# Performance work log

Measured on AMD Instinct MI355X. Metric: run time of the kernel, lower is better.

## Reference

```python
import jax, jax.numpy as jnp
import numpy as np

N, E, G, D, FIN, L, ELAB = 150000, 600000, 8192, 128, 16, 4, 500000
BN_EPS = 1e-5


def _bn(h, g, b, rm, rv):
    # eval-mode BatchNorm1d with running stats
    return (h - rm) * g * jax.lax.rsqrt(rv + BN_EPS) + b


def _pool_max(h, batch):
    # global_max_pool; empty segments -> 0 (instead of -inf)
    p = jax.ops.segment_max(h, batch, num_segments=G)
    return jnp.where(jnp.isneginf(p), 0.0, p)


def setup_inputs() -> dict:
    key = jax.random.key(0)
    ks = jax.random.split(key, 24)
    s_in = 1.0 / np.sqrt(FIN)
    s_d = 1.0 / np.sqrt(D)
    inp = {
        "x": jax.random.normal(ks[0], (N, FIN), jnp.float32),
        "edge_index": jax.random.randint(ks[1], (2, E), 0, N, jnp.int32),
        "batch": jnp.sort(jax.random.randint(ks[2], (N,), 0, G, jnp.int32)),
        "edge_index_labeled": jax.random.randint(ks[3], (2, ELAB), 0, G, jnp.int32),
        "edge_label": jax.random.randint(ks[4], (ELAB,), 0, 2, jnp.int32),
        # initial node encoder + initial linear (num_classes == emb_sizes == D)
        "enc_W": jax.random.normal(ks[5], (FIN, D), jnp.float32) * s_in,
        "enc_b": jnp.zeros((D,), jnp.float32),
        "init_W": jax.random.normal(ks[6], (D, D), jnp.float32) * s_d,
        "init_b": jnp.zeros((D,), jnp.float32),
        # per-layer GIN params (stacked over L layers)
        "gin_eps": jnp.zeros((L,), jnp.float32),
        "W1": jax.random.normal(ks[7], (L, D, D), jnp.float32) * s_d,
        "b1": jnp.zeros((L, D), jnp.float32),
        "g1": jnp.ones((L, D), jnp.float32),
        "be1": jnp.zeros((L, D), jnp.float32),
        "rm1": jnp.zeros((L, D), jnp.float32),
        "rv1": jnp.ones((L, D), jnp.float32),
        "W2": jax.random.normal(ks[8], (L, D, D), jnp.float32) * s_d,
        "b2": jnp.zeros((L, D), jnp.float32),
        "g2": jnp.ones((L, D), jnp.float32),
        "be2": jnp.zeros((L, D), jnp.float32),
        "rm2": jnp.zeros((L, D), jnp.float32),
        "rv2": jnp.ones((L, D), jnp.float32),
        # per-layer linear applied to pooled features
        "lin_W": jax.random.normal(ks[9], (L, D, D), jnp.float32) * s_d,
        "lin_b": jnp.zeros((L, D), jnp.float32),
        # layer_post_mp: ReLU -> Linear(D,D) -> ReLU -> Linear(D,1)
        "post_W1": jax.random.normal(ks[10], (D, D), jnp.float32) * s_d,
        "post_b1": jnp.zeros((D,), jnp.float32),
        "post_W2": jax.random.normal(ks[11], (D, 1), jnp.float32) * s_d,
        "post_b2": jnp.zeros((1,), jnp.float32),
    }
    return inp


def reference(x, edge_index, batch, edge_index_labeled, edge_label,
              enc_W, enc_b, init_W, init_b, gin_eps,
              W1, b1, g1, be1, rm1, rv1,
              W2, b2, g2, be2, rm2, rv2,
              lin_W, lin_b, post_W1, post_b1, post_W2, post_b2):
    src, dst = edge_index[0], edge_index[1]

    # initial MLP (node encoder) -> [N, D]
    x_feat = x @ enc_W + enc_b

    # out = dropout(pool(initial_linear(x_feat)))  (dropout = identity, eval)
    out = _pool_max(x_feat @ init_W + init_b, batch)  # [G, D]

    for i in range(L):
        # GINConv: mlp((1 + eps) * x + sum_{j in N(i)} x_j)
        agg = jax.ops.segment_sum(x_feat[src], dst, num_segments=N)  # [N, D]
        h = (1.0 + gin_eps[i]) * x_feat + agg
        h = jax.nn.relu(_bn(h @ W1[i] + b1[i], g1[i], be1[i], rm1[i], rv1[i]))
        x_feat = jax.nn.relu(_bn(h @ W2[i] + b2[i], g2[i], be2[i], rm2[i], rv2[i]))
        # out += dropout(linear(pool(x_feat)))
        out = out + (_pool_max(x_feat, batch) @ lin_W[i] + lin_b[i])

    # layer_post_mp: ReLU -> Linear -> ReLU -> Linear(D,1)
    out = jax.nn.relu(out)
    out = jax.nn.relu(out @ post_W1 + post_b1)
    out = out @ post_W2 + post_b2  # [G, 1]

    # _apply_index gather + dot-product decode
    pred_pairs = out[edge_index_labeled]  # [2, ELAB, 1]
    pred = jnp.sum(pred_pairs[0] * pred_pairs[1], axis=-1)  # [ELAB]
    return pred, edge_label
```

## Files before the change

kernel.cpp:

```cpp
#include <hip/hip_runtime.h>

#define NN 150000
#define NP 150016
#define NE 600000
#define NG 8192
#define DD 128
#define FINN 16
#define NL 4
#define NEL 500000
#define BN_EPS 1e-5f
#define NB_SCAN 147

typedef __attribute__((ext_vector_type(8))) short bf16x8;
typedef __attribute__((ext_vector_type(4))) float f32x4;
typedef __attribute__((ext_vector_type(2))) float f32x2;

__device__ inline short bfr(float x) {
    unsigned u = __builtin_bit_cast(unsigned, x);
    unsigned r = u + 0x7fffu + ((u >> 16) & 1u);
    return (short)(r >> 16);
}
__device__ inline float bf2f(short h) {
    return __builtin_bit_cast(float, ((unsigned)(unsigned short)h) << 16);
}

__global__ __launch_bounds__(256) void enc_kernel(const float* __restrict__ x,
                                                  const float* __restrict__ W,
                                                  const float* __restrict__ b,
                                                  float* __restrict__ out) {
    int t = threadIdx.x;
    int c4 = (t & 31) * 4;
    float4 wreg[16];
#pragma unroll
    for (int k = 0; k < 16; k++) wreg[k] = *(const float4*)&W[k * DD + c4];
    float4 bias = *(const float4*)&b[c4];
    int rbase = blockIdx.x * 128 + (t >> 5);
#pragma unroll
    for (int it = 0; it < 16; it++) {
        int row = rbase + it * 8;
        if (row >= NN) break;
        const float4* xr = (const float4*)(x + (size_t)row * FINN);
        float4 x0 = xr[0], x1 = xr[1], x2 = xr[2], x3 = xr[3];
        float xs[16] = {x0.x, x0.y, x0.z, x0.w, x1.x, x1.y, x1.z, x1.w,
                        x2.x, x2.y, x2.z, x2.w, x3.x, x3.y, x3.z, x3.w};
        float4 acc = bias;
#pragma unroll
        for (int k = 0; k < 16; k++) {
            acc.x += xs[k] * wreg[k].x;
            acc.y += xs[k] * wreg[k].y;
            acc.z += xs[k] * wreg[k].z;
            acc.w += xs[k] * wreg[k].w;
        }
        *(float4*)&out[(size_t)row * DD + c4] = acc;
    }
}

__global__ void prep_w_kernel(const float* __restrict__ initW, const float* __restrict__ W1,
                              const float* __restrict__ W2, bf16x8* __restrict__ Wph,
                              bf16x8* __restrict__ Wpl) {
    int tid = blockIdx.x * 256 + threadIdx.x;
    if (tid >= 9 * 2048) return;
    int mat = tid >> 11;
    int rem = tid & 2047;
    int kk = rem >> 9;
    int c = (rem >> 6) & 7;
    int lane = rem & 63;
    const float* Wm;
    if (mat == 0) Wm = initW;
    else if (mat <= 4) Wm = W1 + (size_t)(mat - 1) * DD * DD;
    else Wm = W2 + (size_t)(mat - 5) * DD * DD;
    int col = c * 16 + (lane & 15);
    int kbase = kk * 32 + (lane >> 4) * 8;
    bf16x8 oh, ol;
#pragma unroll
    for (int j = 0; j < 8; j++) {
        float v = Wm[(size_t)(kbase + j) * DD + col];
        short h = bfr(v);
        oh[j] = h;
        ol[j] = bfr(v - bf2f(h));
    }
    Wph[tid] = oh;
    Wpl[tid] = ol;
}

__global__ void prep_scb_kernel(const float* __restrict__ initb,
                                const float* __restrict__ b1, const float* __restrict__ g1,
                                const float* __restrict__ be1, const float* __restrict__ rm1,
                                const float* __restrict__ rv1,
                                const float* __restrict__ b2, const float* __restrict__ g2,
                                const float* __restrict__ be2, const float* __restrict__ rm2,
                                const float* __restrict__ rv2,
                                float* __restrict__ sc, float* __restrict__ bb) {
    int tid = blockIdx.x * 256 + threadIdx.x;
    if (tid >= 9 * DD) return;
    int mat = tid >> 7, d = tid & 127;
    float s, o;
    if (mat == 0) {
        s = 1.f;
        o = initb[d];
    } else {
        const float *b_, *g_, *be_, *rm_, *rv_;
        int i;
        if (mat <= 4) { i = mat - 1; b_ = b1; g_ = g1; be_ = be1; rm_ = rm1; rv_ = rv1; }
        else          { i = mat - 5; b_ = b2; g_ = g2; be_ = be2; rm_ = rm2; rv_ = rv2; }
        float t = g_[i * DD + d] * rsqrtf(rv_[i * DD + d] + BN_EPS);
        s = t;
        o = (b_[i * DD + d] - rm_[i * DD + d]) * t + be_[i * DD + d];
    }
    sc[tid] = s;
    bb[tid] = o;
}

__global__ void zero_int_kernel(int* __restrict__ p, int n) {
    int i = blockIdx.x * 256 + threadIdx.x;
    if (i < n) p[i] = 0;
}

__global__ void hist_kernel(const int* __restrict__ dst, int* __restrict__ deg) {
    int e = blockIdx.x * 256 + threadIdx.x;
    if (e < NE) atomicAdd(&deg[dst[e]], 1);
}

__global__ void scan_reduce_kernel(const int* __restrict__ deg, int* __restrict__ bsum) {
    __shared__ int s[256];
    int b = blockIdx.x, t = threadIdx.x;
    int base = b * 1024 + t * 4;
    int v = 0;
#pragma unroll
    for (int i = 0; i < 4; i++) {
        int idx = base + i;
        if (idx < NN) v += deg[idx];
    }
    s[t] = v;
    __syncthreads();
    for (int off = 128; off > 0; off >>= 1) {
        if (t < off) s[t] += s[t + off];
        __syncthreads();
    }
    if (t == 0) bsum[b] = s[0];
}

__global__ void scan_mid_kernel(const int* __restrict__ bsum, int* __restrict__ boff,
                                int* __restrict__ rowptrN) {
    __shared__ int s[256];
    int t = threadIdx.x;
    int v = (t < NB_SCAN) ? bsum[t] : 0;
    s[t] = v;
    __syncthreads();
    for (int off = 1; off < 256; off <<= 1) {
        int u = (t >= off) ? s[t - off] : 0;
        __syncthreads();
        s[t] += u;
        __syncthreads();
    }
    if (t < NB_SCAN) boff[t] = s[t] - v;
    if (t == 255) *rowptrN = s[255];
}

__global__ void scan_final_kernel(const int* __restrict__ deg, const int* __restrict__ boff,
                                  int* __restrict__ rowptr) {
    __shared__ int s[256];
    int b = blockIdx.x, t = threadIdx.x;
    int base = b * 1024 + t * 4;
    int v[4];
    int sum = 0;
#pragma unroll
    for (int i = 0; i < 4; i++) {
        int idx = base + i;
        v[i] = (idx < NN) ? deg[idx] : 0;
        sum += v[i];
    }
    s[t] = sum;
    __syncthreads();
    int my = sum;
    for (int off = 1; off < 256; off <<= 1) {
        int u = (t >= off) ? s[t - off] : 0;
        __syncthreads();
        s[t] += u;
        __syncthreads();
    }
    int excl = s[t] - my + boff[b];
#pragma unroll
    for (int i = 0; i < 4; i++) {
        int idx = base + i;
        if (idx < NN) rowptr[idx] = excl;
        excl += v[i];
    }
}

__global__ void copy_int_kernel(const int* __restrict__ a, int* __restrict__ b, int n) {
    int i = blockIdx.x * 256 + threadIdx.x;
    if (i < n) b[i] = a[i];
}

__global__ void fill_kernel(const int* __restrict__ src, const int* __restrict__ dst,
                            int* cursor, int* __restrict__ csr_src) {
    int e = blockIdx.x * 256 + threadIdx.x;
    if (e >= NE) return;
    int p = atomicAdd(&cursor[dst[e]], 1);
    csr_src[p] = src[e];
}

__global__ void gstart_kernel(const int* __restrict__ batch, int* __restrict__ gstart) {
    int n = blockIdx.x * 256 + threadIdx.x;
    if (n >= NN) return;
    int b = batch[n];
    int prev = (n == 0) ? -1 : batch[n - 1];
    for (int g = prev + 1; g <= b; g++) gstart[g] = n;
    if (n == NN - 1) {
        for (int g = b + 1; g <= NG; g++) gstart[g] = NN;
    }
}

__global__ __launch_bounds__(256) void agg_kernel(const float* __restrict__ A,
                                                  const int* __restrict__ rowptr,
                                                  const int* __restrict__ csr_src,
                                                  const float* __restrict__ gin_eps,
                                                  int li, unsigned short* __restrict__ Bh) {
    int n = __builtin_amdgcn_readfirstlane(blockIdx.x * 4 + (threadIdx.x >> 6));
    int c2 = (threadIdx.x & 63) * 2;
    float e1 = 1.f + gin_eps[li];
    int s = __builtin_amdgcn_readfirstlane(rowptr[n]);
    int e = __builtin_amdgcn_readfirstlane(rowptr[n + 1]);
    f32x2 acc = *(const f32x2*)&A[(size_t)n * DD + c2] * e1;
    int i = s;
    for (; i + 8 <= e; i += 8) {
        int j0 = __builtin_amdgcn_readfirstlane(csr_src[i + 0]);
        int j1 = __builtin_amdgcn_readfirstlane(csr_src[i + 1]);
        int j2 = __builtin_amdgcn_readfirstlane(csr_src[i + 2]);
        int j3 = __builtin_amdgcn_readfirstlane(csr_src[i + 3]);
        int j4 = __builtin_amdgcn_readfirstlane(csr_src[i + 4]);
        int j5 = __builtin_amdgcn_readfirstlane(csr_src[i + 5]);
        int j6 = __builtin_amdgcn_readfirstlane(csr_src[i + 6]);
        int j7 = __builtin_amdgcn_readfirstlane(csr_src[i + 7]);
        f32x2 v0 = *(const f32x2*)&A[(size_t)j0 * DD + c2];
        f32x2 v1 = *(const f32x2*)&A[(size_t)j1 * DD + c2];
        f32x2 v2 = *(const f32x2*)&A[(size_t)j2 * DD + c2];
        f32x2 v3 = *(const f32x2*)&A[(size_t)j3 * DD + c2];
        f32x2 v4 = *(const f32x2*)&A[(size_t)j4 * DD + c2];
        f32x2 v5 = *(const f32x2*)&A[(size_t)j5 * DD + c2];
        f32x2 v6 = *(const f32x2*)&A[(size_t)j6 * DD + c2];
        f32x2 v7 = *(const f32x2*)&A[(size_t)j7 * DD + c2];
        acc += ((v0 + v1) + (v2 + v3)) + ((v4 + v5) + (v6 + v7));
    }
    if (i + 4 <= e) {
        int j0 = __builtin_amdgcn_readfirstlane(csr_src[i + 0]);
        int j1 = __builtin_amdgcn_readfirstlane(csr_src[i + 1]);
        int j2 = __builtin_amdgcn_readfirstlane(csr_src[i + 2]);
        int j3 = __builtin_amdgcn_readfirstlane(csr_src[i + 3]);
        f32x2 v0 = *(const f32x2*)&A[(size_t)j0 * DD + c2];
        f32x2 v1 = *(const f32x2*)&A[(size_t)j1 * DD + c2];
        f32x2 v2 = *(const f32x2*)&A[(size_t)j2 * DD + c2];
        f32x2 v3 = *(const f32x2*)&A[(size_t)j3 * DD + c2];
        acc += (v0 + v1) + (v2 + v3);
        i += 4;
    }
    for (; i < e; i++) {
        int j = __builtin_amdgcn_readfirstlane(csr_src[i]);
        acc += *(const f32x2*)&A[(size_t)j * DD + c2];
    }
    unsigned lo = (unsigned)(unsigned short)bfr(acc[0]);
    unsigned hi = (unsigned)(unsigned short)bfr(acc[1]);
    *(unsigned*)&Bh[(size_t)n * DD + c2] = lo | (hi << 16);
}

template <int RELU>
__global__ __launch_bounds__(256) void mm_kernel(const float* __restrict__ A,
                                                 float* __restrict__ C,
                                                 const bf16x8* __restrict__ Wph,
                                                 const bf16x8* __restrict__ Wpl,
                                                 const float* __restrict__ sc,
                                                 const float* __restrict__ bb) {
    int lane = threadIdx.x & 63;
    int wid = threadIdx.x >> 6;
    int row0 = blockIdx.x * 128 + wid * 32;
    int r16 = lane & 15;
    int kg = lane >> 4;
    f32x4 acc[2][8];
#pragma unroll
    for (int m = 0; m < 2; m++)
#pragma unroll
        for (int c = 0; c < 8; c++) acc[m][c] = (f32x4){0.f, 0.f, 0.f, 0.f};
#pragma unroll
    for (int kk = 0; kk < 4; kk++) {
        bf16x8 ah[2], al[2];
#pragma unroll
        for (int m = 0; m < 2; m++) {
            const float* ap = A + (size_t)(row0 + m * 16 + r16) * DD + kk * 32 + kg * 8;
            float4 lo = *(const float4*)ap;
            float4 hi = *(const float4*)(ap + 4);
            float v[8] = {lo.x, lo.y, lo.z, lo.w, hi.x, hi.y, hi.z, hi.w};
            bf16x8 th, tl;
#pragma unroll
            for (int j = 0; j < 8; j++) {
                short h = bfr(v[j]);
                th[j] = h;
                tl[j] = bfr(v[j] - bf2f(h));
            }
            ah[m] = th;
            al[m] = tl;
        }
#pragma unroll
        for (int c = 0; c < 8; c++) {
            bf16x8 wh = Wph[kk * 512 + c * 64 + lane];
            bf16x8 wl = Wpl[kk * 512 + c * 64 + lane];
#pragma unroll
            for (int m = 0; m < 2; m++) {
                acc[m][c] = __builtin_amdgcn_mfma_f32_16x16x32_bf16(ah[m], wh, acc[m][c], 0, 0, 0);
                acc[m][c] = __builtin_amdgcn_mfma_f32_16x16x32_bf16(al[m], wh, acc[m][c], 0, 0, 0);
                acc[m][c] = __builtin_amdgcn_mfma_f32_16x16x32_bf16(ah[m], wl, acc[m][c], 0, 0, 0);
            }
        }
    }
#pragma unroll
    for (int c = 0; c < 8; c++) {
        int col = c * 16 + r16;
        float s = sc[col], o = bb[col];
#pragma unroll
        for (int m = 0; m < 2; m++) {
            int rbase = row0 + m * 16 + kg * 4;
#pragma unroll
            for (int j = 0; j < 4; j++) {
                int row = rbase + j;
                if (row < NN) {
                    float v = acc[m][c][j] * s + o;
                    if (RELU) v = fmaxf(v, 0.f);
                    C[(size_t)row * DD + col] = v;
                }
            }
        }
    }
}

__global__ __launch_bounds__(256) void mm2x_kernel(
    const unsigned short* __restrict__ Bh, float* __restrict__ Aout,
    const bf16x8* __restrict__ Wph1, const bf16x8* __restrict__ Wpl1,
    const bf16x8* __restrict__ Wph2, const bf16x8* __restrict__ Wpl2,
    const float* __restrict__ sc1, const float* __restrict__ bb1,
    const float* __restrict__ sc2, const float* __restrict__ bb2) {
    __shared__ float hl[128 * 128];
    int lane = threadIdx.x & 63;
    int wid = threadIdx.x >> 6;
    int row0 = blockIdx.x * 128 + wid * 32;
    int r16 = lane & 15;
    int kg = lane >> 4;
    f32x4 acc[2][8];
#pragma unroll
    for (int m = 0; m < 2; m++)
#pragma unroll
        for (int c = 0; c < 8; c++) acc[m][c] = (f32x4){0.f, 0.f, 0.f, 0.f};

#pragma unroll
    for (int kk = 0; kk < 4; kk++) {
        bf16x8 ab[2];
#pragma unroll
        for (int m = 0; m < 2; m++) {
            ab[m] = *(const bf16x8*)&Bh[(size_t)(row0 + m * 16 + r16) * DD + kk * 32 + kg * 8];
        }
#pragma unroll
        for (int c = 0; c < 8; c++) {
            bf16x8 wh = Wph1[kk * 512 + c * 64 + lane];
            bf16x8 wl = Wpl1[kk * 512 + c * 64 + lane];
#pragma unroll
            for (int m = 0; m < 2; m++) {
                acc[m][c] = __builtin_amdgcn_mfma_f32_16x16x32_bf16(ab[m], wh, acc[m][c], 0, 0, 0);
                acc[m][c] = __builtin_amdgcn_mfma_f32_16x16x32_bf16(ab[m], wl, acc[m][c], 0, 0, 0);
            }
        }
    }
#pragma unroll
    for (int c = 0; c < 8; c++) {
        int col = c * 16 + r16;
        float s = sc1[col], o = bb1[col];
#pragma unroll
        for (int m = 0; m < 2; m++) {
#pragma unroll
            for (int j = 0; j < 4; j++) {
                int rl = wid * 32 + m * 16 + kg * 4 + j;
                float v = fmaxf(acc[m][c][j] * s + o, 0.f);
                hl[rl * 128 + (col ^ ((rl & 7) << 2))] = v;
            }
        }
    }
    __syncthreads();

#pragma unroll
    for (int m = 0; m < 2; m++)
#pragma unroll
        for (int c = 0; c < 8; c++) acc[m][c] = (f32x4){0.f, 0.f, 0.f, 0.f};
#pragma unroll
    for (int kk = 0; kk < 4; kk++) {
        bf16x8 ah[2], al[2];
#pragma unroll
        for (int m = 0; m < 2; m++) {
            int rl = wid * 32 + m * 16 + r16;
            int sw = (rl & 7) << 2;
            int c0 = kk * 32 + kg * 8;
            float4 lo = *(const float4*)&hl[rl * 128 + (c0 ^ sw)];
            float4 hi = *(const float4*)&hl[rl * 128 + ((c0 + 4) ^ sw)];
            float v[8] = {lo.x, lo.y, lo.z, lo.w, hi.x, hi.y, hi.z, hi.w};
            bf16x8 th, tl;
#pragma unroll
            for (int j = 0; j < 8; j++) {
                short h = bfr(v[j]);
                th[j] = h;
                tl[j] = bfr(v[j] - bf2f(h));
            }
            ah[m] = th;
            al[m] = tl;
        }
#pragma unroll
        for (int c = 0; c < 8; c++) {
            bf16x8 wh = Wph2[kk * 512 + c * 64 + lane];
            bf16x8 wl = Wpl2[kk * 512 + c * 64 + lane];
#pragma unroll
            for (int m = 0; m < 2; m++) {
                acc[m][c] = __builtin_amdgcn_mfma_f32_16x16x32_bf16(ah[m], wh, acc[m][c], 0, 0, 0);
                acc[m][c] = __builtin_amdgcn_mfma_f32_16x16x32_bf16(al[m], wh, acc[m][c], 0, 0, 0);
                acc[m][c] = __builtin_amdgcn_mfma_f32_16x16x32_bf16(ah[m], wl, acc[m][c], 0, 0, 0);
            }
        }
    }
#pragma unroll
    for (int c = 0; c < 8; c++) {
        int col = c * 16 + r16;
        float s = sc2[col], o = bb2[col];
#pragma unroll
        for (int m = 0; m < 2; m++) {
            int rbase = row0 + m * 16 + kg * 4;
#pragma unroll
            for (int j = 0; j < 4; j++) {
                int row = rbase + j;
                if (row < NN) {
                    Aout[(size_t)row * DD + col] = fmaxf(acc[m][c][j] * s + o, 0.f);
                }
            }
        }
    }
}

__global__ void pool0_kernel(const float* __restrict__ X, const int* __restrict__ gstart,
                             float* __restrict__ OUT) {
    int gph = blockIdx.x;
    int d = threadIdx.x;
    int start = gstart[gph], end = gstart[gph + 1];
    float m;
    if (start >= end) {
        m = 0.f;
    } else {
        m = -INFINITY;
        for (int n = start; n < end; n++) m = fmaxf(m, X[(size_t)n * DD + d]);
    }
    OUT[(size_t)gph * DD + d] = m;
}

__global__ __launch_bounds__(128) void poollin_kernel(const float* __restrict__ X,
                                                      const int* __restrict__ gstart,
                                                      const float* __restrict__ W,
                                                      const float* __restrict__ b,
                                                      float* __restrict__ OUT) {
    __shared__ float p[4][DD];
    int g0 = blockIdx.x * 4;
    int d = threadIdx.x;
#pragma unroll
    for (int gg = 0; gg < 4; gg++) {
        int start = gstart[g0 + gg], end = gstart[g0 + gg + 1];
        float m;
        if (start >= end) {
            m = 0.f;
        } else {
            m = -INFINITY;
            for (int n = start; n < end; n++) m = fmaxf(m, X[(size_t)n * DD + d]);
        }
        p[gg][d] = m;
    }
    __syncthreads();
    float acc0 = b[d], acc1 = b[d], acc2 = b[d], acc3 = b[d];
#pragma unroll 8
    for (int k = 0; k < DD; k++) {
        float w = W[k * DD + d];
        acc0 += p[0][k] * w;
        acc1 += p[1][k] * w;
        acc2 += p[2][k] * w;
        acc3 += p[3][k] * w;
    }
    OUT[(size_t)(g0 + 0) * DD + d] += acc0;
    OUT[(size_t)(g0 + 1) * DD + d] += acc1;
    OUT[(size_t)(g0 + 2) * DD + d] += acc2;
    OUT[(size_t)(g0 + 3) * DD + d] += acc3;
}

__global__ void post_kernel(const float* __restrict__ OUT, const float* __restrict__ W1,
                            const float* __restrict__ b1, const float* __restrict__ W2,
                            const float* __restrict__ b2, float* __restrict__ S) {
    __shared__ float o[DD];
    __shared__ float red[2];
    int gph = blockIdx.x, d = threadIdx.x;
    o[d] = fmaxf(OUT[(size_t)gph * DD + d], 0.f);
    __syncthreads();
    float acc = b1[d];
#pragma unroll 8
    for (int k = 0; k < DD; k++) acc += o[k] * W1[k * DD + d];
    acc = fmaxf(acc, 0.f);
    float v = acc * W2[d];
#pragma unroll
    for (int off = 32; off > 0; off >>= 1) v += __shfl_down(v, off);
    if ((d & 63) == 0) red[d >> 6] = v;
    __syncthreads();
    if (d == 0) S[gph] = red[0] + red[1] + b2[0];
}

__global__ void pred_kernel(const int* __restrict__ eil, const int* __restrict__ el,
                            const float* __restrict__ S, float* __restrict__ out) {
    int i = blockIdx.x * blockDim.x + threadIdx.x;
    if (i >= NEL) return;
    int a = eil[i], b = eil[NEL + i];
    out[i] = S[a] * S[b];
    out[NEL + i] = (float)el[i];
}

extern "C" void kernel_launch(void* const* d_in, const int* in_sizes, int n_in,
                              void* d_out, int out_size, void* d_ws, size_t ws_size,
                              hipStream_t stream) {
    const float* x = (const float*)d_in[0];
    const int* edge_index = (const int*)d_in[1];
    const int* batch = (const int*)d_in[2];
    const int* eil = (const int*)d_in[3];
    const int* el = (const int*)d_in[4];
    const float* encW = (const float*)d_in[5];
    const float* encb = (const float*)d_in[6];
    const float* initW = (const float*)d_in[7];
    const float* initb = (const float*)d_in[8];
    const float* gin_eps = (const float*)d_in[9];
    const float* W1 = (const float*)d_in[10];
    const float* b1 = (const float*)d_in[11];
    const float* g1 = (const float*)d_in[12];
    const float* be1 = (const float*)d_in[13];
    const float* rm1 = (const float*)d_in[14];
    const float* rv1 = (const float*)d_in[15];
    const float* W2 = (const float*)d_in[16];
    const float* b2 = (const float*)d_in[17];
    const float* g2 = (const float*)d_in[18];
    const float* be2 = (const float*)d_in[19];
    const float* rm2 = (const float*)d_in[20];
    const float* rv2 = (const float*)d_in[21];
    const float* linW = (const float*)d_in[22];
    const float* linb = (const float*)d_in[23];
    const float* postW1 = (const float*)d_in[24];
    const float* postb1 = (const float*)d_in[25];
    const float* postW2 = (const float*)d_in[26];
    const float* postb2 = (const float*)d_in[27];

    const int* srcArr = edge_index;
    const int* dstArr = edge_index + NE;

    char* w = (char*)d_ws;
    auto carve = [&](size_t bytes) -> char* {
        char* p = w;
        w += (bytes + 255) & ~(size_t)255;
        return p;
    };
    float* A = (float*)carve((size_t)NP * DD * 4);
    float* B = (float*)carve((size_t)NP * DD * 4);
    float* OUTb = (float*)carve((size_t)NG * DD * 4);
    float* S = (float*)carve((size_t)NG * 4);
    int* deg = (int*)carve((size_t)NN * 4);
    int* rowptr = (int*)carve((size_t)(NN + 1) * 4);
    int* cursor = (int*)carve((size_t)NN * 4);
    int* csr_src = (int*)carve((size_t)NE * 4);
    int* bsum = (int*)carve((size_t)NB_SCAN * 4);
    int* boff = (int*)carve((size_t)NB_SCAN * 4);
    int* gstart = (int*)carve((size_t)(NG + 1) * 4);
    bf16x8* Wph = (bf16x8*)carve((size_t)9 * 2048 * 16);
    bf16x8* Wpl = (bf16x8*)carve((size_t)9 * 2048 * 16);
    float* scv = (float*)carve((size_t)9 * DD * 4);
    float* bbv = (float*)carve((size_t)9 * DD * 4);

    unsigned short* Bh = (unsigned short*)B;

    float* out = (float*)d_out;
    const int mmBlk = NP / 128;

    prep_w_kernel<<<72, 256, 0, stream>>>(initW, W1, W2, Wph, Wpl);
    prep_scb_kernel<<<5, 256, 0, stream>>>(initb, b1, g1, be1, rm1, rv1,
                                           b2, g2, be2, rm2, rv2, scv, bbv);

    zero_int_kernel<<<586, 256, 0, stream>>>(deg, NN);
    hist_kernel<<<2344, 256, 0, stream>>>(dstArr, deg);
    scan_reduce_kernel<<<NB_SCAN, 256, 0, stream>>>(deg, bsum);
    scan_mid_kernel<<<1, 256, 0, stream>>>(bsum, boff, rowptr + NN);
    scan_final_kernel<<<NB_SCAN, 256, 0, stream>>>(deg, boff, rowptr);
    copy_int_kernel<<<586, 256, 0, stream>>>(rowptr, cursor, NN);
    fill_kernel<<<2344, 256, 0, stream>>>(srcArr, dstArr, cursor, csr_src);
    gstart_kernel<<<586, 256, 0, stream>>>(batch, gstart);

    enc_kernel<<<mmBlk, 256, 0, stream>>>(x, encW, encb, A);
    mm_kernel<0><<<mmBlk, 256, 0, stream>>>(A, B, Wph, Wpl, scv, bbv);
    pool0_kernel<<<NG, DD, 0, stream>>>(B, gstart, OUTb);

    for (int i = 0; i < NL; i++) {
        agg_kernel<<<NN / 4, 256, 0, stream>>>(A, rowptr, csr_src, gin_eps, i, Bh);
        mm2x_kernel<<<mmBlk, 256, 0, stream>>>(
            Bh, A,
            Wph + (size_t)(1 + i) * 2048, Wpl + (size_t)(1 + i) * 2048,
            Wph + (size_t)(5 + i) * 2048, Wpl + (size_t)(5 + i) * 2048,
            scv + (1 + i) * DD, bbv + (1 + i) * DD,
            scv + (5 + i) * DD, bbv + (5 + i) * DD);
        poollin_kernel<<<NG / 4, DD, 0, stream>>>(A, gstart, linW + (size_t)i * DD * DD,
                                                  linb + i * DD, OUTb);
    }

    post_kernel<<<NG, DD, 0, stream>>>(OUTb, postW1, postb1, postW2, postb2, S);
    pred_kernel<<<(NEL + 255) / 256, 256, 0, stream>>>(eil, el, S, out);
}
```

Before: 1.007 ms.

## Store node feature buffers in bf16 instead of fp32 across all kernels

Node activation buffers (encoder output, layer outputs, init-linear output) are now stored as bf16 rather than fp32. The gather-aggregate, matmul and pooling kernels read and unpack bf16, and the first matmul drops the hi/lo split of activations. This halves the memory traffic for the gather-heavy aggregation and the pooling reads. The cost is lower precision in stored activations and in the max-pool inputs, which may affect accuracy against tolerance.

```diff
diff --git a/kernel.cpp b/kernel.cpp
--- a/kernel.cpp
+++ b/kernel.cpp
@@ -13,7 +13,6 @@
 
 typedef __attribute__((ext_vector_type(8))) short bf16x8;
 typedef __attribute__((ext_vector_type(4))) float f32x4;
-typedef __attribute__((ext_vector_type(2))) float f32x2;
 
 __device__ inline short bfr(float x) {
     unsigned u = __builtin_bit_cast(unsigned, x);
@@ -23,11 +22,14 @@
 __device__ inline float bf2f(short h) {
     return __builtin_bit_cast(float, ((unsigned)(unsigned short)h) << 16);
 }
+__device__ inline unsigned pack2(float a, float b) {
+    return (unsigned)(unsigned short)bfr(a) | ((unsigned)(unsigned short)bfr(b) << 16);
+}
 
 __global__ __launch_bounds__(256) void enc_kernel(const float* __restrict__ x,
                                                   const float* __restrict__ W,
                                                   const float* __restrict__ b,
-                                                  float* __restrict__ out) {
+                                                  unsigned short* __restrict__ out) {
     int t = threadIdx.x;
     int c4 = (t & 31) * 4;
     float4 wreg[16];
@@ -51,7 +53,10 @@
             acc.z += xs[k] * wreg[k].z;
             acc.w += xs[k] * wreg[k].w;
         }
-        *(float4*)&out[(size_t)row * DD + c4] = acc;
+        uint2 pk;
+        pk.x = pack2(acc.x, acc.y);
+        pk.y = pack2(acc.z, acc.w);
+        *(uint2*)&out[(size_t)row * DD + c4] = pk;
     }
 }
 
@@ -212,7 +217,7 @@
     }
 }
 
-__global__ __launch_bounds__(256) void agg_kernel(const float* __restrict__ A,
+__global__ __launch_bounds__(256) void agg_kernel(const unsigned short* __restrict__ A,
                                                   const int* __restrict__ rowptr,
                                                   const int* __restrict__ csr_src,
                                                   const float* __restrict__ gin_eps,
@@ -222,7 +227,9 @@
     float e1 = 1.f + gin_eps[li];
     int s = __builtin_amdgcn_readfirstlane(rowptr[n]);
     int e = __builtin_amdgcn_readfirstlane(rowptr[n + 1]);
-    f32x2 acc = *(const f32x2*)&A[(size_t)n * DD + c2] * e1;
+    unsigned u = *(const unsigned*)&A[(size_t)n * DD + c2];
+    float acc0 = bf2f((short)(u & 0xffff)) * e1;
+    float acc1 = bf2f((short)(u >> 16)) * e1;
     int i = s;
     for (; i + 8 <= e; i += 8) {
         int j0 = __builtin_amdgcn_readfirstlane(csr_src[i + 0]);
@@ -233,44 +240,53 @@
         int j5 = __builtin_amdgcn_readfirstlane(csr_src[i + 5]);
         int j6 = __builtin_amdgcn_readfirstlane(csr_src[i + 6]);
         int j7 = __builtin_amdgcn_readfirstlane(csr_src[i + 7]);
-        f32x2 v0 = *(const f32x2*)&A[(size_t)j0 * DD + c2];
-        f32x2 v1 = *(const f32x2*)&A[(size_t)j1 * DD + c2];
-        f32x2 v2 = *(const f32x2*)&A[(size_t)j2 * DD + c2];
-        f32x2 v3 = *(const f32x2*)&A[(size_t)j3 * DD + c2];
-        f32x2 v4 = *(const f32x2*)&A[(size_t)j4 * DD + c2];
-        f32x2 v5 = *(const f32x2*)&A[(size_t)j5 * DD + c2];
-        f32x2 v6 = *(const f32x2*)&A[(size_t)j6 * DD + c2];
-        f32x2 v7 = *(const f32x2*)&A[(size_t)j7 * DD + c2];
-        acc += ((v0 + v1) + (v2 + v3)) + ((v4 + v5) + (v6 + v7));
+        unsigned u0 = *(const unsigned*)&A[(size_t)j0 * DD + c2];
+        unsigned u1 = *(const unsigned*)&A[(size_t)j1 * DD + c2];
+        unsigned u2 = *(const unsigned*)&A[(size_t)j2 * DD + c2];
+        unsigned u3 = *(const unsigned*)&A[(size_t)j3 * DD + c2];
+        unsigned u4 = *(const unsigned*)&A[(size_t)j4 * DD + c2];
+        unsigned u5 = *(const unsigned*)&A[(size_t)j5 * DD + c2];
+        unsigned u6 = *(const unsigned*)&A[(size_t)j6 * DD + c2];
+        unsigned u7 = *(const unsigned*)&A[(size_t)j7 * DD + c2];
+        acc0 += ((bf2f((short)(u0 & 0xffff)) + bf2f((short)(u1 & 0xffff))) +
+                 (bf2f((short)(u2 & 0xffff)) + bf2f((short)(u3 & 0xffff)))) +
+                ((bf2f((short)(u4 & 0xffff)) + bf2f((short)(u5 & 0xffff))) +
+                 (bf2f((short)(u6 & 0xffff)) + bf2f((short)(u7 & 0xffff))));
+        acc1 += ((bf2f((short)(u0 >> 16)) + bf2f((short)(u1 >> 16))) +
+                 (bf2f((short)(u2 >> 16)) + bf2f((short)(u3 >> 16)))) +
+                ((bf2f((short)(u4 >> 16)) + bf2f((short)(u5 >> 16))) +
+                 (bf2f((short)(u6 >> 16)) + bf2f((short)(u7 >> 16))));
     }
     if (i + 4 <= e) {
         int j0 = __builtin_amdgcn_readfirstlane(csr_src[i + 0]);
         int j1 = __builtin_amdgcn_readfirstlane(csr_src[i + 1]);
         int j2 = __builtin_amdgcn_readfirstlane(csr_src[i + 2]);
         int j3 = __builtin_amdgcn_readfirstlane(csr_src[i + 3]);
-        f32x2 v0 = *(const f32x2*)&A[(size_t)j0 * DD + c2];
-        f32x2 v1 = *(const f32x2*)&A[(size_t)j1 * DD + c2];
-        f32x2 v2 = *(const f32x2*)&A[(size_t)j2 * DD + c2];
-        f32x2 v3 = *(const f32x2*)&A[(size_t)j3 * DD + c2];
-        acc += (v0 + v1) + (v2 + v3);
+        unsigned u0 = *(const unsigned*)&A[(size_t)j0 * DD + c2];
+        unsigned u1 = *(const unsigned*)&A[(size_t)j1 * DD + c2];
+        unsigned u2 = *(const unsigned*)&A[(size_t)j2 * DD + c2];
+        unsigned u3 = *(const unsigned*)&A[(size_t)j3 * DD + c2];
+        acc0 += (bf2f((short)(u0 & 0xffff)) + bf2f((short)(u1 & 0xffff))) +
+                (bf2f((short)(u2 & 0xffff)) + bf2f((short)(u3 & 0xffff)));
+        acc1 += (bf2f((short)(u0 >> 16)) + bf2f((short)(u1 >> 16))) +
+                (bf2f((short)(u2 >> 16)) + bf2f((short)(u3 >> 16)));
         i += 4;
     }
     for (; i < e; i++) {
         int j = __builtin_amdgcn_readfirstlane(csr_src[i]);
-        acc += *(const f32x2*)&A[(size_t)j * DD + c2];
-    }
-    unsigned lo = (unsigned)(unsigned short)bfr(acc[0]);
-    unsigned hi = (unsigned)(unsigned short)bfr(acc[1]);
-    *(unsigned*)&Bh[(size_t)n * DD + c2] = lo | (hi << 16);
-}
-
-template <int RELU>
-__global__ __launch_bounds__(256) void mm_kernel(const float* __restrict__ A,
-                                                 float* __restrict__ C,
-                                                 const bf16x8* __restrict__ Wph,
-                                                 const bf16x8* __restrict__ Wpl,
-                                                 const float* __restrict__ sc,
-                                                 const float* __restrict__ bb) {
+        unsigned uj = *(const unsigned*)&A[(size_t)j * DD + c2];
+        acc0 += bf2f((short)(uj & 0xffff));
+        acc1 += bf2f((short)(uj >> 16));
+    }
+    *(unsigned*)&Bh[(size_t)n * DD + c2] = pack2(acc0, acc1);
+}
+
+__global__ __launch_bounds__(256) void mm0_kernel(const unsigned short* __restrict__ Ah,
+                                                  unsigned short* __restrict__ C,
+                                                  const bf16x8* __restrict__ Wph,
+                                                  const bf16x8* __restrict__ Wpl,
+                                                  const float* __restrict__ sc,
+                                                  const float* __restrict__ bb) {
     int lane = threadIdx.x & 63;
     int wid = threadIdx.x >> 6;
     int row0 = blockIdx.x * 128 + wid * 32;
@@ -283,32 +299,18 @@
         for (int c = 0; c < 8; c++) acc[m][c] = (f32x4){0.f, 0.f, 0.f, 0.f};
 #pragma unroll
     for (int kk = 0; kk < 4; kk++) {
-        bf16x8 ah[2], al[2];
-#pragma unroll
-        for (int m = 0; m < 2; m++) {
-            const float* ap = A + (size_t)(row0 + m * 16 + r16) * DD + kk * 32 + kg * 8;
-            float4 lo = *(const float4*)ap;
-            float4 hi = *(const float4*)(ap + 4);
-            float v[8] = {lo.x, lo.y, lo.z, lo.w, hi.x, hi.y, hi.z, hi.w};
-            bf16x8 th, tl;
-#pragma unroll
-            for (int j = 0; j < 8; j++) {
-                short h = bfr(v[j]);
-                th[j] = h;
-                tl[j] = bfr(v[j] - bf2f(h));
-            }
-            ah[m] = th;
-            al[m] = tl;
-        }
+        bf16x8 ab[2];
+#pragma unroll
+        for (int m = 0; m < 2; m++)
+            ab[m] = *(const bf16x8*)&Ah[(size_t)(row0 + m * 16 + r16) * DD + kk * 32 + kg * 8];
 #pragma unroll
         for (int c = 0; c < 8; c++) {
             bf16x8 wh = Wph[kk * 512 + c * 64 + lane];
             bf16x8 wl = Wpl[kk * 512 + c * 64 + lane];
 #pragma unroll
             for (int m = 0; m < 2; m++) {
-                acc[m][c] = __builtin_amdgcn_mfma_f32_16x16x32_bf16(ah[m], wh, acc[m][c], 0, 0, 0);
-                acc[m][c] = __builtin_amdgcn_mfma_f32_16x16x32_bf16(al[m], wh, acc[m][c], 0, 0, 0);
-                acc[m][c] = __builtin_amdgcn_mfma_f32_16x16x32_bf16(ah[m], wl, acc[m][c], 0, 0, 0);
+                acc[m][c] = __builtin_amdgcn_mfma_f32_16x16x32_bf16(ab[m], wh, acc[m][c], 0, 0, 0);
+                acc[m][c] = __builtin_amdgcn_mfma_f32_16x16x32_bf16(ab[m], wl, acc[m][c], 0, 0, 0);
             }
         }
     }
@@ -322,18 +324,15 @@
 #pragma unroll
             for (int j = 0; j < 4; j++) {
                 int row = rbase + j;
-                if (row < NN) {
-                    float v = acc[m][c][j] * s + o;
-                    if (RELU) v = fmaxf(v, 0.f);
-                    C[(size_t)row * DD + col] = v;
-                }
+                if (row < NN)
+                    C[(size_t)row * DD + col] = (unsigned short)bfr(acc[m][c][j] * s + o);
             }
         }
     }
 }
 
 __global__ __launch_bounds__(256) void mm2x_kernel(
-    const unsigned short* __restrict__ Bh, float* __restrict__ Aout,
+    const unsigned short* __restrict__ Bh, unsigned short* __restrict__ Aout,
     const bf16x8* __restrict__ Wph1, const bf16x8* __restrict__ Wpl1,
     const bf16x8* __restrict__ Wph2, const bf16x8* __restrict__ Wpl2,
     const float* __restrict__ sc1, const float* __restrict__ bb1,
@@ -354,9 +353,8 @@
     for (int kk = 0; kk < 4; kk++) {
         bf16x8 ab[2];
 #pragma unroll
-        for (int m = 0; m < 2; m++) {
+        for (int m = 0; m < 2; m++)
             ab[m] = *(const bf16x8*)&Bh[(size_t)(row0 + m * 16 + r16) * DD + kk * 32 + kg * 8];
-        }
 #pragma unroll
         for (int c = 0; c < 8; c++) {
             bf16x8 wh = Wph1[kk * 512 + c * 64 + lane];
@@ -431,16 +429,16 @@
 #pragma unroll
             for (int j = 0; j < 4; j++) {
                 int row = rbase + j;
-                if (row < NN) {
-                    Aout[(size_t)row * DD + col] = fmaxf(acc[m][c][j] * s + o, 0.f);
-                }
+                if (row < NN)
+                    Aout[(size_t)row * DD + col] =
+                        (unsigned short)bfr(fmaxf(acc[m][c][j] * s + o, 0.f));
             }
         }
     }
 }
 
-__global__ void pool0_kernel(const float* __restrict__ X, const int* __restrict__ gstart,
-                             float* __restrict__ OUT) {
+__global__ void pool0_kernel(const unsigned short* __restrict__ X,
+                             const int* __restrict__ gstart, float* __restrict__ OUT) {
     int gph = blockIdx.x;
     int d = threadIdx.x;
     int start = gstart[gph], end = gstart[gph + 1];
@@ -449,12 +447,13 @@
         m = 0.f;
     } else {
         m = -INFINITY;
-        for (int n = start; n < end; n++) m = fmaxf(m, X[(size_t)n * DD + d]);
+        for (int n = start; n < end; n++)
+            m = fmaxf(m, bf2f((short)X[(size_t)n * DD + d]));
     }
     OUT[(size_t)gph * DD + d] = m;
 }
 
-__global__ __launch_bounds__(128) void poollin_kernel(const float* __restrict__ X,
+__global__ __launch_bounds__(128) void poollin_kernel(const unsigned short* __restrict__ X,
                                                       const int* __restrict__ gstart,
                                                       const float* __restrict__ W,
                                                       const float* __restrict__ b,
@@ -470,7 +469,8 @@
             m = 0.f;
         } else {
             m = -INFINITY;
-            for (int n = start; n < end; n++) m = fmaxf(m, X[(size_t)n * DD + d]);
+            for (int n = start; n < end; n++)
+                m = fmaxf(m, bf2f((short)X[(size_t)n * DD + d]));
         }
         p[gg][d] = m;
     }
@@ -560,8 +560,8 @@
         w += (bytes + 255) & ~(size_t)255;
         return p;
     };
-    float* A = (float*)carve((size_t)NP * DD * 4);
-    float* B = (float*)carve((size_t)NP * DD * 4);
+    unsigned short* A = (unsigned short*)carve((size_t)NP * DD * 2);
+    unsigned short* Bh = (unsigned short*)carve((size_t)NP * DD * 2);
     float* OUTb = (float*)carve((size_t)NG * DD * 4);
     float* S = (float*)carve((size_t)NG * 4);
     int* deg = (int*)carve((size_t)NN * 4);
@@ -576,8 +576,6 @@
     float* scv = (float*)carve((size_t)9 * DD * 4);
     float* bbv = (float*)carve((size_t)9 * DD * 4);
 
-    unsigned short* Bh = (unsigned short*)B;
-
     float* out = (float*)d_out;
     const int mmBlk = NP / 128;
 
@@ -595,8 +593,8 @@
     gstart_kernel<<<586, 256, 0, stream>>>(batch, gstart);
 
     enc_kernel<<<mmBlk, 256, 0, stream>>>(x, encW, encb, A);
-    mm_kernel<0><<<mmBlk, 256, 0, stream>>>(A, B, Wph, Wpl, scv, bbv);
-    pool0_kernel<<<NG, DD, 0, stream>>>(B, gstart, OUTb);
+    mm0_kernel<<<mmBlk, 256, 0, stream>>>(A, Bh, Wph, Wpl, scv, bbv);
+    pool0_kernel<<<NG, DD, 0, stream>>>(Bh, gstart, OUTb);
 
     for (int i = 0; i < NL; i++) {
         agg_kernel<<<NN / 4, 256, 0, stream>>>(A, rowptr, csr_src, gin_eps, i, Bh);
```

New measurement: 898.2 us. -10.8%, faster.
